# Kernel tuning notes

Hardware: AMD Instinct MI355X
Metric: run time of the kernel (lower is better)

Reference implementation:

```python
import jax, jax.numpy as jnp
import numpy as np

K = 1024  # num_points to sample (matches init_kwargs)


def setup_inputs() -> dict:
    key = jax.random.key(0)
    k1, k2 = jax.random.split(key)
    B, N, C = 16, 100000, 16
    points = jax.random.normal(k1, (B, N, C), dtype=jnp.float32)
    start_idx = jax.random.randint(k2, (B,), 0, N, dtype=jnp.int32)
    return {"points": points, "start_idx": start_idx}


def _sample_farthest_points(xyz, start_idx, k):
    # xyz: [B, N, 3], start_idx: [B] int32. Returns idx: [B, k] int32.
    B, N, _ = xyz.shape

    def body(carry, _):
        min_d, last = carry                                    # [B,N], [B]
        sel = jnp.take_along_axis(xyz, last[:, None, None], axis=1)  # [B,1,3]
        d = jnp.sum((xyz - sel) ** 2, axis=-1)                 # [B,N]
        min_d = jnp.minimum(min_d, d)
        nxt = jnp.argmax(min_d, axis=-1).astype(jnp.int32)     # [B]
        return (min_d, nxt), last

    init = (jnp.full((B, N), jnp.inf, dtype=xyz.dtype), start_idx)
    _, idx = jax.lax.scan(body, init, None, length=k)          # idx: [k, B]
    return idx.T                                               # [B, k]


def reference(points, start_idx):
    # Faithful 'fps' strategy: farthest point sampling on xyz, gather all channels.
    xyz = points[:, :, :3].astype(jnp.float32)
    idx = _sample_farthest_points(xyz, start_idx, K)           # [B, K]
    out = jnp.take_along_axis(points, idx[:, :, None], axis=1) # [B, K, C]
    return out
```

## Files before the change

kernel.cpp:

```cpp
#include <hip/hip_runtime.h>

#define NB    16
#define NPTS  100000
#define NCH   16
#define KSEL  1024
#define SLOTS 16
#define TPB   256
#define CHUNK 6250
#define PPT   25
#define MAGA  0x19u
#define MAGB  0x13u

typedef unsigned long long u64;
typedef unsigned int u32;


__device__ __forceinline__ void combine(float ov, int oi, float& v, int& i) {
  if (ov > v || (ov == v && oi < i)) { v = ov; i = oi; }
}

__global__ __launch_bounds__(TPB, 1)
void fps_kernel(const float* __restrict__ points, const int* __restrict__ start_idx,
                u64* __restrict__ ws_cand, int* __restrict__ ws_idx) {
  const int raw  = blockIdx.x;
  const int xcd  = raw & 7;
  const int s    = raw >> 3;
  const int b    = xcd + 8 * (s >> 4);
  const int slot = s & 15;

  const int tid  = threadIdx.x;
  const int lane = tid & 63;
  const int wid  = tid >> 6;

  const int base = slot * CHUNK;
  const float* __restrict__ pb = points + (size_t)b * NPTS * NCH;

  float px[PPT], py[PPT], pz[PPT], md[PPT];
  #pragma unroll
  for (int k = 0; k < PPT; ++k) {
    const int li = tid + (k << 8);
    const bool valid = li < CHUNK;
    float4 p = make_float4(0.f, 0.f, 0.f, 0.f);
    if (valid) p = *reinterpret_cast<const float4*>(pb + (size_t)(base + li) * NCH);
    px[k] = p.x; py[k] = p.y; pz[k] = p.z;
    md[k] = valid ? __builtin_inff() : -__builtin_inff();
  }
  #pragma unroll
  for (int k = 0; k < PPT; ++k)
    asm volatile("" : "+v"(px[k]), "+v"(py[k]), "+v"(pz[k]), "+v"(md[k]));

  __shared__ float s_rv[4];
  __shared__ int   s_ri[4];
  __shared__ float s_wx, s_wy, s_wz;

  const int sidx = start_idx[b];
  float sx, sy, sz;
  {
    const float4 p = *reinterpret_cast<const float4*>(pb + (size_t)sidx * NCH);
    sx = p.x; sy = p.y; sz = p.z;
  }
  if (slot == 0 && tid == 0) ws_idx[b * KSEL] = sidx;

  for (int i = 0; i < KSEL - 1; ++i) {
    const int par = i & 1;
    u64* const blk = ws_cand + (((size_t)par * NB + b) << 6);

    float bv = -__builtin_inff();
    int   bi = 0x7fffffff;
    #pragma unroll
    for (int k = 0; k < PPT; ++k) {
      const float dx = __fsub_rn(px[k], sx);
      const float dy = __fsub_rn(py[k], sy);
      const float dz = __fsub_rn(pz[k], sz);
      const float d  = __fadd_rn(__fadd_rn(__fmul_rn(dx, dx), __fmul_rn(dy, dy)),
                                 __fmul_rn(dz, dz));
      const float m  = fminf(md[k], d);
      md[k] = m;
      if (m > bv) { bv = m; bi = base + tid + (k << 8); }
    }

    #pragma unroll
    for (int m = 32; m >= 1; m >>= 1) {
      const float ov = __shfl_xor(bv, m, 64);
      const int   oi = __shfl_xor(bi, m, 64);
      combine(ov, oi, bv, bi);
    }
    if (lane == 0) { s_rv[wid] = bv; s_ri[wid] = bi; }
    __syncthreads();

    bv = s_rv[0]; bi = s_ri[0];
    #pragma unroll
    for (int w = 1; w < 4; ++w) combine(s_rv[w], s_ri[w], bv, bi);

    const u32 tm = (u32)(i + 1) << 5;

    const int local = bi - base;
    if (tid == (local & 255)) {
      const int kk = local >> 8;
      float ox = 0.f, oy = 0.f, oz = 0.f;
      #pragma unroll
      for (int k = 0; k < PPT; ++k)
        if (k == kk) { ox = px[k]; oy = py[k]; oz = pz[k]; }
      const u32 inv  = 131071u - (u32)bi;
      const u32 loA  = (inv << 15) | tm | MAGA;
      const u32 loB  = (inv << 15) | tm | MAGB;
      __hip_atomic_store(blk      + slot, ((u64)__float_as_uint(bv) << 32) | loA,
                         __ATOMIC_RELAXED, __HIP_MEMORY_SCOPE_AGENT);
      __hip_atomic_store(blk + 16 + slot, ((u64)__float_as_uint(ox) << 32) | loB,
                         __ATOMIC_RELAXED, __HIP_MEMORY_SCOPE_AGENT);
      __hip_atomic_store(blk + 32 + slot, ((u64)__float_as_uint(oy) << 32) | loB,
                         __ATOMIC_RELAXED, __HIP_MEMORY_SCOPE_AGENT);
      __hip_atomic_store(blk + 48 + slot, ((u64)__float_as_uint(oz) << 32) | loB,
                         __ATOMIC_RELAXED, __HIP_MEMORY_SCOPE_AGENT);
    }

    if (wid == 0) {
      const int wrd = lane >> 4;
      const u64* const myp = blk + lane;
      const u32 want = tm | (wrd == 0 ? MAGA : MAGB);
      u64 q;
      for (;;) {
        q = __hip_atomic_load(myp, __ATOMIC_RELAXED, __HIP_MEMORY_SCOPE_AGENT);
        if (__all(((u32)q & 0x7FFFu) == want)) break;
        __builtin_amdgcn_s_sleep(1);
      }
      u64 key = q;
      #pragma unroll
      for (int m = 8; m >= 1; m >>= 1) {
        const u64 o = __shfl_xor(key, m, 64);
        if (o > key) key = o;
      }
      const u64 kmax = __shfl(key, 0, 64);
      const unsigned long long ball = __ballot(wrd == 0 && q == kmax);
      const int rs = __ffsll(ball) - 1;
      const u32 xb = (u32)__shfl((int)(u32)(q >> 32), 16 + rs, 64);
      const u32 yb = (u32)__shfl((int)(u32)(q >> 32), 32 + rs, 64);
      const u32 zb = (u32)__shfl((int)(u32)(q >> 32), 48 + rs, 64);
      if (lane == 0) {
        s_wx = __uint_as_float(xb);
        s_wy = __uint_as_float(yb);
        s_wz = __uint_as_float(zb);
        if (slot == 0)
          ws_idx[b * KSEL + i + 1] = 131071 - (int)((kmax >> 15) & 0x1FFFFu);
      }
    }
    __syncthreads();
    sx = s_wx; sy = s_wy; sz = s_wz;
  }
}

__global__ void gather_kernel(const float* __restrict__ points,
                              const int* __restrict__ ws_idx,
                              float* __restrict__ out) {
  const int e = blockIdx.x * TPB + threadIdx.x;
  const int c = e & 15;
  const int k = (e >> 4) & (KSEL - 1);
  const int b = e >> 14;
  const int idx = ws_idx[b * KSEL + k];
  out[e] = points[((size_t)b * NPTS + idx) * NCH + c];
}

extern "C" void kernel_launch(void* const* d_in, const int* in_sizes, int n_in,
                              void* d_out, int out_size, void* d_ws, size_t ws_size,
                              hipStream_t stream) {
  const float* points    = (const float*)d_in[0];
  const int*   start_idx = (const int*)d_in[1];
  float*       out       = (float*)d_out;

  u64* cand = (u64*)((char*)d_ws + 4096);
  int* idxl = (int*)((char*)d_ws + 65536);

  hipMemsetAsync(cand, 0, 2 * NB * 4 * SLOTS * sizeof(u64), stream);

  fps_kernel<<<NB * SLOTS, TPB, 0, stream>>>(points, start_idx, cand, idxl);
  gather_kernel<<<(NB * KSEL * NCH) / TPB, TPB, 0, stream>>>(points, idxl, out);
}
```

Baseline: 2.858 ms.

## Halve blocks per batch and broadcast candidates to per-reader rows

Each batch now uses 8 blocks of 512 threads instead of 16 blocks of 256, so fewer blocks take part in the per-iteration cross-block exchange. Every writer now pushes its candidate record into a separate row for each reader block, so a reader polls one contiguous 32-word row. The sleep in the spin loop is removed to cut wake-up latency. In exchange there are 8x more atomic stores per iteration and busier polling, the XCD-aware block mapping is dropped, and fewer blocks are resident (128 instead of 256).

```diff
diff --git a/kernel.cpp b/kernel.cpp
--- a/kernel.cpp
+++ b/kernel.cpp
@@ -4,9 +4,9 @@
 #define NPTS  100000
 #define NCH   16
 #define KSEL  1024
-#define SLOTS 16
-#define TPB   256
-#define CHUNK 6250
+#define SLOTS 8
+#define TPB   512
+#define CHUNK 12500
 #define PPT   25
 #define MAGA  0x19u
 #define MAGB  0x13u
@@ -23,10 +23,8 @@
 void fps_kernel(const float* __restrict__ points, const int* __restrict__ start_idx,
                 u64* __restrict__ ws_cand, int* __restrict__ ws_idx) {
   const int raw  = blockIdx.x;
-  const int xcd  = raw & 7;
-  const int s    = raw >> 3;
-  const int b    = xcd + 8 * (s >> 4);
-  const int slot = s & 15;
+  const int b    = raw >> 3;
+  const int slot = raw & 7;
 
   const int tid  = threadIdx.x;
   const int lane = tid & 63;
@@ -38,7 +36,7 @@
   float px[PPT], py[PPT], pz[PPT], md[PPT];
   #pragma unroll
   for (int k = 0; k < PPT; ++k) {
-    const int li = tid + (k << 8);
+    const int li = tid + (k << 9);
     const bool valid = li < CHUNK;
     float4 p = make_float4(0.f, 0.f, 0.f, 0.f);
     if (valid) p = *reinterpret_cast<const float4*>(pb + (size_t)(base + li) * NCH);
@@ -49,8 +47,8 @@
   for (int k = 0; k < PPT; ++k)
     asm volatile("" : "+v"(px[k]), "+v"(py[k]), "+v"(pz[k]), "+v"(md[k]));
 
-  __shared__ float s_rv[4];
-  __shared__ int   s_ri[4];
+  __shared__ float s_rv[8];
+  __shared__ int   s_ri[8];
   __shared__ float s_wx, s_wy, s_wz;
 
   const int sidx = start_idx[b];
@@ -63,7 +61,7 @@
 
   for (int i = 0; i < KSEL - 1; ++i) {
     const int par = i & 1;
-    u64* const blk = ws_cand + (((size_t)par * NB + b) << 6);
+    u64* const bblk = ws_cand + (((size_t)par * NB + b) << 8);
 
     float bv = -__builtin_inff();
     int   bi = 0x7fffffff;
@@ -76,7 +74,7 @@
                                  __fmul_rn(dz, dz));
       const float m  = fminf(md[k], d);
       md[k] = m;
-      if (m > bv) { bv = m; bi = base + tid + (k << 8); }
+      if (m > bv) { bv = m; bi = base + tid + (k << 9); }
     }
 
     #pragma unroll
@@ -90,52 +88,57 @@
 
     bv = s_rv[0]; bi = s_ri[0];
     #pragma unroll
-    for (int w = 1; w < 4; ++w) combine(s_rv[w], s_ri[w], bv, bi);
+    for (int w = 1; w < 8; ++w) combine(s_rv[w], s_ri[w], bv, bi);
 
     const u32 tm = (u32)(i + 1) << 5;
 
     const int local = bi - base;
-    if (tid == (local & 255)) {
-      const int kk = local >> 8;
+    if (tid == (local & 511)) {
+      const int kk = local >> 9;
       float ox = 0.f, oy = 0.f, oz = 0.f;
       #pragma unroll
       for (int k = 0; k < PPT; ++k)
         if (k == kk) { ox = px[k]; oy = py[k]; oz = pz[k]; }
-      const u32 inv  = 131071u - (u32)bi;
-      const u32 loA  = (inv << 15) | tm | MAGA;
-      const u32 loB  = (inv << 15) | tm | MAGB;
-      __hip_atomic_store(blk      + slot, ((u64)__float_as_uint(bv) << 32) | loA,
-                         __ATOMIC_RELAXED, __HIP_MEMORY_SCOPE_AGENT);
-      __hip_atomic_store(blk + 16 + slot, ((u64)__float_as_uint(ox) << 32) | loB,
-                         __ATOMIC_RELAXED, __HIP_MEMORY_SCOPE_AGENT);
-      __hip_atomic_store(blk + 32 + slot, ((u64)__float_as_uint(oy) << 32) | loB,
-                         __ATOMIC_RELAXED, __HIP_MEMORY_SCOPE_AGENT);
-      __hip_atomic_store(blk + 48 + slot, ((u64)__float_as_uint(oz) << 32) | loB,
-                         __ATOMIC_RELAXED, __HIP_MEMORY_SCOPE_AGENT);
+      const u32 inv = 131071u - (u32)bi;
+      const u64 w0 = ((u64)__float_as_uint(bv) << 32) | (inv << 15) | tm | MAGA;
+      const u64 meta = (u64)((inv << 15) | tm | MAGB);
+      const u64 w1 = ((u64)__float_as_uint(ox) << 32) | meta;
+      const u64 w2 = ((u64)__float_as_uint(oy) << 32) | meta;
+      const u64 w3 = ((u64)__float_as_uint(oz) << 32) | meta;
+      #pragma unroll
+      for (int r = 0; r < SLOTS; ++r) {
+        u64* const rec = bblk + (((size_t)r << 5) + ((size_t)slot << 2));
+        __hip_atomic_store(rec + 0, w0, __ATOMIC_RELAXED, __HIP_MEMORY_SCOPE_AGENT);
+        __hip_atomic_store(rec + 1, w1, __ATOMIC_RELAXED, __HIP_MEMORY_SCOPE_AGENT);
+        __hip_atomic_store(rec + 2, w2, __ATOMIC_RELAXED, __HIP_MEMORY_SCOPE_AGENT);
+        __hip_atomic_store(rec + 3, w3, __ATOMIC_RELAXED, __HIP_MEMORY_SCOPE_AGENT);
+      }
     }
 
     if (wid == 0) {
-      const int wrd = lane >> 4;
-      const u64* const myp = blk + lane;
-      const u32 want = tm | (wrd == 0 ? MAGA : MAGB);
-      u64 q;
+      const u64* const row = bblk + ((size_t)slot << 5);
+      const bool active = lane < 32;
+      const int  word   = lane & 3;
+      const u32  want   = tm | (word == 0 ? MAGA : MAGB);
+      u64 q = 0;
       for (;;) {
-        q = __hip_atomic_load(myp, __ATOMIC_RELAXED, __HIP_MEMORY_SCOPE_AGENT);
-        if (__all(((u32)q & 0x7FFFu) == want)) break;
-        __builtin_amdgcn_s_sleep(1);
+        if (active) q = __hip_atomic_load(row + lane, __ATOMIC_RELAXED, __HIP_MEMORY_SCOPE_AGENT);
+        const bool ok = !active || (((u32)q & 0x7FFFu) == want);
+        if (__all(ok)) break;
       }
-      u64 key = q;
+      u64 key = (active && word == 0) ? q : 0;
       #pragma unroll
-      for (int m = 8; m >= 1; m >>= 1) {
+      for (int m = 4; m <= 16; m <<= 1) {
         const u64 o = __shfl_xor(key, m, 64);
         if (o > key) key = o;
       }
       const u64 kmax = __shfl(key, 0, 64);
-      const unsigned long long ball = __ballot(wrd == 0 && q == kmax);
-      const int rs = __ffsll(ball) - 1;
-      const u32 xb = (u32)__shfl((int)(u32)(q >> 32), 16 + rs, 64);
-      const u32 yb = (u32)__shfl((int)(u32)(q >> 32), 32 + rs, 64);
-      const u32 zb = (u32)__shfl((int)(u32)(q >> 32), 48 + rs, 64);
+      const unsigned long long ball = __ballot(active && word == 0 && q == kmax);
+      const int wl = __ffsll(ball) - 1;
+      const u32 hi = (u32)(q >> 32);
+      const u32 xb = (u32)__shfl((int)hi, wl + 1, 64);
+      const u32 yb = (u32)__shfl((int)hi, wl + 2, 64);
+      const u32 zb = (u32)__shfl((int)hi, wl + 3, 64);
       if (lane == 0) {
         s_wx = __uint_as_float(xb);
         s_wy = __uint_as_float(yb);
@@ -152,7 +155,7 @@
 __global__ void gather_kernel(const float* __restrict__ points,
                               const int* __restrict__ ws_idx,
                               float* __restrict__ out) {
-  const int e = blockIdx.x * TPB + threadIdx.x;
+  const int e = blockIdx.x * 256 + threadIdx.x;
   const int c = e & 15;
   const int k = (e >> 4) & (KSEL - 1);
   const int b = e >> 14;
@@ -168,10 +171,10 @@
   float*       out       = (float*)d_out;
 
   u64* cand = (u64*)((char*)d_ws + 4096);
-  int* idxl = (int*)((char*)d_ws + 65536);
+  int* idxl = (int*)((char*)d_ws + 131072);
 
-  hipMemsetAsync(cand, 0, 2 * NB * 4 * SLOTS * sizeof(u64), stream);
+  hipMemsetAsync(cand, 0, 2 * NB * SLOTS * SLOTS * 4 * sizeof(u64), stream);
 
   fps_kernel<<<NB * SLOTS, TPB, 0, stream>>>(points, start_idx, cand, idxl);
-  gather_kernel<<<(NB * KSEL * NCH) / TPB, TPB, 0, stream>>>(points, idxl, out);
+  gather_kernel<<<(NB * KSEL * NCH) / 256, 256, 0, stream>>>(points, idxl, out);
 }
```

New measurement: 3.579 ms. 1.25x slower.

## Halve cooperating blocks per batch to eight with larger per-thread point chunks

Applied to the files above, without the earlier changes.

Each batch is now split across 8 blocks instead of 16, and each thread holds 49 points in registers instead of 25. The cross-block candidate exchange and spin-wait reduction shrink to 8 slots, using 32 active lanes. The block-to-batch mapping is simplified and drops the XCD-aware interleaving. The aim is to cut inter-block synchronisation and atomic-exchange overhead per iteration. In exchange, per-block compute per iteration roughly doubles, register pressure rises, and fewer CUs are used.

```diff
diff --git a/kernel.cpp b/kernel.cpp
--- a/kernel.cpp
+++ b/kernel.cpp
@@ -4,10 +4,10 @@
 #define NPTS  100000
 #define NCH   16
 #define KSEL  1024
-#define SLOTS 16
+#define SLOTS 8
 #define TPB   256
-#define CHUNK 6250
-#define PPT   25
+#define CHUNK 12500
+#define PPT   49
 #define MAGA  0x19u
 #define MAGB  0x13u
 
@@ -23,10 +23,8 @@
 void fps_kernel(const float* __restrict__ points, const int* __restrict__ start_idx,
                 u64* __restrict__ ws_cand, int* __restrict__ ws_idx) {
   const int raw  = blockIdx.x;
-  const int xcd  = raw & 7;
-  const int s    = raw >> 3;
-  const int b    = xcd + 8 * (s >> 4);
-  const int slot = s & 15;
+  const int b    = raw >> 3;
+  const int slot = raw & 7;
 
   const int tid  = threadIdx.x;
   const int lane = tid & 63;
@@ -63,7 +61,7 @@
 
   for (int i = 0; i < KSEL - 1; ++i) {
     const int par = i & 1;
-    u64* const blk = ws_cand + (((size_t)par * NB + b) << 6);
+    u64* const blk = ws_cand + (((size_t)par * NB + b) << 5);
 
     float bv = -__builtin_inff();
     int   bi = 0x7fffffff;
@@ -101,41 +99,42 @@
       #pragma unroll
       for (int k = 0; k < PPT; ++k)
         if (k == kk) { ox = px[k]; oy = py[k]; oz = pz[k]; }
-      const u32 inv  = 131071u - (u32)bi;
-      const u32 loA  = (inv << 15) | tm | MAGA;
-      const u32 loB  = (inv << 15) | tm | MAGB;
+      const u32 inv = 131071u - (u32)bi;
+      const u32 loA = (inv << 15) | tm | MAGA;
+      const u32 loB = (inv << 15) | tm | MAGB;
       __hip_atomic_store(blk      + slot, ((u64)__float_as_uint(bv) << 32) | loA,
                          __ATOMIC_RELAXED, __HIP_MEMORY_SCOPE_AGENT);
-      __hip_atomic_store(blk + 16 + slot, ((u64)__float_as_uint(ox) << 32) | loB,
+      __hip_atomic_store(blk +  8 + slot, ((u64)__float_as_uint(ox) << 32) | loB,
                          __ATOMIC_RELAXED, __HIP_MEMORY_SCOPE_AGENT);
-      __hip_atomic_store(blk + 32 + slot, ((u64)__float_as_uint(oy) << 32) | loB,
+      __hip_atomic_store(blk + 16 + slot, ((u64)__float_as_uint(oy) << 32) | loB,
                          __ATOMIC_RELAXED, __HIP_MEMORY_SCOPE_AGENT);
-      __hip_atomic_store(blk + 48 + slot, ((u64)__float_as_uint(oz) << 32) | loB,
+      __hip_atomic_store(blk + 24 + slot, ((u64)__float_as_uint(oz) << 32) | loB,
                          __ATOMIC_RELAXED, __HIP_MEMORY_SCOPE_AGENT);
     }
 
     if (wid == 0) {
-      const int wrd = lane >> 4;
-      const u64* const myp = blk + lane;
-      const u32 want = tm | (wrd == 0 ? MAGA : MAGB);
-      u64 q;
+      const bool active = lane < 32;
+      const int  word   = lane >> 3;
+      const u32  want   = tm | (word == 0 ? MAGA : MAGB);
+      u64 q = 0;
       for (;;) {
-        q = __hip_atomic_load(myp, __ATOMIC_RELAXED, __HIP_MEMORY_SCOPE_AGENT);
-        if (__all(((u32)q & 0x7FFFu) == want)) break;
+        if (active) q = __hip_atomic_load(blk + lane, __ATOMIC_RELAXED, __HIP_MEMORY_SCOPE_AGENT);
+        if (__all(!active || (((u32)q & 0x7FFFu) == want))) break;
         __builtin_amdgcn_s_sleep(1);
       }
-      u64 key = q;
+      u64 key = (active && word == 0) ? q : 0;
       #pragma unroll
-      for (int m = 8; m >= 1; m >>= 1) {
+      for (int m = 4; m >= 1; m >>= 1) {
         const u64 o = __shfl_xor(key, m, 64);
         if (o > key) key = o;
       }
       const u64 kmax = __shfl(key, 0, 64);
-      const unsigned long long ball = __ballot(wrd == 0 && q == kmax);
-      const int rs = __ffsll(ball) - 1;
-      const u32 xb = (u32)__shfl((int)(u32)(q >> 32), 16 + rs, 64);
-      const u32 yb = (u32)__shfl((int)(u32)(q >> 32), 32 + rs, 64);
-      const u32 zb = (u32)__shfl((int)(u32)(q >> 32), 48 + rs, 64);
+      const unsigned long long ball = __ballot(active && word == 0 && q == kmax);
+      const int ws = __ffsll(ball) - 1;
+      const u32 hi = (u32)(q >> 32);
+      const u32 xb = (u32)__shfl((int)hi,  8 + ws, 64);
+      const u32 yb = (u32)__shfl((int)hi, 16 + ws, 64);
+      const u32 zb = (u32)__shfl((int)hi, 24 + ws, 64);
       if (lane == 0) {
         s_wx = __uint_as_float(xb);
         s_wy = __uint_as_float(yb);
@@ -152,7 +151,7 @@
 __global__ void gather_kernel(const float* __restrict__ points,
                               const int* __restrict__ ws_idx,
                               float* __restrict__ out) {
-  const int e = blockIdx.x * TPB + threadIdx.x;
+  const int e = blockIdx.x * 256 + threadIdx.x;
   const int c = e & 15;
   const int k = (e >> 4) & (KSEL - 1);
   const int b = e >> 14;
@@ -173,5 +172,5 @@
   hipMemsetAsync(cand, 0, 2 * NB * 4 * SLOTS * sizeof(u64), stream);
 
   fps_kernel<<<NB * SLOTS, TPB, 0, stream>>>(points, start_idx, cand, idxl);
-  gather_kernel<<<(NB * KSEL * NCH) / TPB, TPB, 0, stream>>>(points, idxl, out);
+  gather_kernel<<<(NB * KSEL * NCH) / 256, 256, 0, stream>>>(points, idxl, out);
 }
```

Result: slower. 3.527 ms (+23.4%).
